# Optimization experiments

Hardware: AMD Instinct MI355X
Metric: run time of the kernel (lower is better)

## Reference

```python
import jax, jax.numpy as jnp
import numpy as np

B, S, D, H = 2, 2048, 1024, 16
HD = D // H  # head_dim = 64


def setup_inputs() -> dict:
    key = jax.random.key(0)
    ks = jax.random.split(key, 5)
    scale = 1.0 / np.sqrt(D)  # xavier-ish init scale
    return {
        "x": jax.random.normal(ks[0], (B, S, D), jnp.float32),
        "Wq": jax.random.normal(ks[1], (D, D), jnp.float32) * scale,
        "Wk": jax.random.normal(ks[2], (D, D), jnp.float32) * scale,
        "Wv": jax.random.normal(ks[3], (D, D), jnp.float32) * scale,
        "Wo": jax.random.normal(ks[4], (D, D), jnp.float32) * scale,
        "bo": jnp.zeros((D,), jnp.float32),
    }


def reference(x, Wq, Wk, Wv, Wo, bo):
    # nn.Linear stores weight as [out, in]; y = x @ W.T
    b, s, d = x.shape
    def heads(t):
        return t.reshape(b, s, H, HD).transpose(0, 2, 1, 3)  # [B,H,S,HD]
    Q = heads(x @ Wq.T)
    K = heads(x @ Wk.T)
    V = heads(x @ Wv.T)
    # Chunked loop in the original sees all K per Q-chunk => full attention.
    scores = jnp.einsum("bhqd,bhkd->bhqk", Q, K) / np.sqrt(HD)
    attn = jax.nn.softmax(scores, axis=-1)
    out = jnp.einsum("bhqk,bhkd->bhqd", attn, V)
    out = out.transpose(0, 2, 1, 3).reshape(b, s, d)
    return out @ Wo.T + bo
```

## Files before the change

kernel.cpp:

```cpp
#include <hip/hip_runtime.h>
#include <hip/hip_bf16.h>
#include <math.h>

#define Bc 2
#define Sc 2048
#define Dc 1024
#define Hc 16
#define HDc 64
#define Mc (Bc*Sc)

using f32x4  = __attribute__((ext_vector_type(4))) float;
using bf16x8 = __attribute__((ext_vector_type(8))) short;
using s16x4  = __attribute__((ext_vector_type(4))) short;
using uint4v = __attribute__((ext_vector_type(4))) unsigned int;

#define GAS(p) ((const __attribute__((address_space(1))) void*)(p))
#define LAS(p) ((__attribute__((address_space(3))) void*)(p))

#define QSC 0.18033688011112042f

__device__ __forceinline__ short f2b(float f) {
  union { float f; unsigned u; } v; v.f = f;
  unsigned r = (v.u + 0x7fffu + ((v.u >> 16) & 1u)) >> 16;
  return (short)r;
}

__global__ __launch_bounds__(256) void cvt_kernel(const float* __restrict__ in,
                                                  short* __restrict__ out, int n4) {
  int i = blockIdx.x * 256 + threadIdx.x;
  if (i >= n4) return;
  float4 v = reinterpret_cast<const float4*>(in)[i];
  s16x4 o;
  o.x = f2b(v.x); o.y = f2b(v.y); o.z = f2b(v.z); o.w = f2b(v.w);
  reinterpret_cast<s16x4*>(out)[i] = o;
}

__global__ __launch_bounds__(256) void cvtw_kernel(
    const float* __restrict__ w0, const float* __restrict__ w1,
    const float* __restrict__ w2, const float* __restrict__ w3,
    short* __restrict__ o0, short* __restrict__ o1,
    short* __restrict__ o2, short* __restrict__ o3) {
  const int sel = blockIdx.y;
  const float* in = (sel == 0) ? w0 : (sel == 1) ? w1 : (sel == 2) ? w2 : w3;
  short* out = (sel == 0) ? o0 : (sel == 1) ? o1 : (sel == 2) ? o2 : o3;
  int i = blockIdx.x * 256 + threadIdx.x;
  float4 v = reinterpret_cast<const float4*>(in)[i];
  s16x4 o;
  o.x = f2b(v.x); o.y = f2b(v.y); o.z = f2b(v.z); o.w = f2b(v.w);
  reinterpret_cast<s16x4*>(out)[i] = o;
}

__device__ __forceinline__ void gemm_core_128(
    const short* __restrict__ A, const short* __restrict__ Bt,
    int m0, int n0, short* As, short* Bs, f32x4 (&acc)[4][4]) {
  const int tid = threadIdx.x;
  const int l = tid & 63;
  const int w = tid >> 6;
  const int wr = w >> 1, wc = w & 1;
  const int g = l >> 4;

  int srow[4], scol[4];
#pragma unroll
  for (int i = 0; i < 4; ++i) {
    int off = w * 1024 + i * 4096 + l * 16;
    int row = off >> 7;
    srow[i] = row;
    scol[i] = (off & 127) ^ ((row & 7) << 4);
  }
  const int rA = (wr * 64 + (l & 15)) * 128;
  const int rB = (wc * 64 + (l & 15)) * 128;
  const int sw = (l & 7) << 4;

  for (int kt = 0; kt < 16; ++kt) {
#pragma unroll
    for (int i = 0; i < 4; ++i) {
      const char* ga = (const char*)A + (size_t)(m0 + srow[i]) * 2048 + kt * 128 + scol[i];
      const char* gb = (const char*)Bt + (size_t)(n0 + srow[i]) * 2048 + kt * 128 + scol[i];
      __builtin_amdgcn_global_load_lds(GAS(ga), LAS((char*)As + w * 1024 + i * 4096), 16, 0, 0);
      __builtin_amdgcn_global_load_lds(GAS(gb), LAS((char*)Bs + w * 1024 + i * 4096), 16, 0, 0);
    }
    __syncthreads();
#pragma unroll
    for (int ks = 0; ks < 2; ++ks) {
      bf16x8 af[4], bfr[4];
#pragma unroll
      for (int mi = 0; mi < 4; ++mi)
        af[mi] = *(const bf16x8*)((const char*)As + rA + mi * 2048 + ((g * 16 + ks * 64) ^ sw));
#pragma unroll
      for (int ni = 0; ni < 4; ++ni)
        bfr[ni] = *(const bf16x8*)((const char*)Bs + rB + ni * 2048 + ((g * 16 + ks * 64) ^ sw));
#pragma unroll
      for (int mi = 0; mi < 4; ++mi)
#pragma unroll
        for (int ni = 0; ni < 4; ++ni)
          acc[mi][ni] = __builtin_amdgcn_mfma_f32_16x16x32_bf16(af[mi], bfr[ni], acc[mi][ni], 0, 0, 0);
    }
    __syncthreads();
  }
}

__global__ __launch_bounds__(256) void qkv_kernel(
    const short* __restrict__ xb, const short* __restrict__ wq,
    const short* __restrict__ wk, const short* __restrict__ wv,
    short* __restrict__ Qb, short* __restrict__ Kb, short* __restrict__ Vb) {
  __shared__ short As[128 * 64];
  __shared__ short Bs[128 * 64];
  const int mt = blockIdx.x, yb = blockIdx.y;
  const int sel = yb >> 3, nb = yb & 7;
  const short* Wt = (sel == 0) ? wq : (sel == 1) ? wk : wv;
  short* Ob = (sel == 0) ? Qb : (sel == 1) ? Kb : Vb;
  const float oscale = (sel == 0) ? QSC : 1.0f;
  f32x4 acc[4][4];
#pragma unroll
  for (int i = 0; i < 4; ++i)
#pragma unroll
    for (int j = 0; j < 4; ++j)
#pragma unroll
      for (int r = 0; r < 4; ++r) acc[i][j][r] = 0.0f;
  gemm_core_128(xb, Wt, mt * 128, nb * 128, As, Bs, acc);
  const int l = threadIdx.x & 63, w = threadIdx.x >> 6;
  const int wr = w >> 1, wc = w & 1, g = l >> 4;
#pragma unroll
  for (int mi = 0; mi < 4; ++mi)
#pragma unroll
    for (int ni = 0; ni < 4; ++ni) {
      int n = nb * 128 + wc * 64 + ni * 16 + (l & 15);
      int h = n >> 6, hd = n & 63;
#pragma unroll
      for (int r = 0; r < 4; ++r) {
        int m = mt * 128 + wr * 64 + mi * 16 + g * 4 + r;
        int b = m >> 11, s = m & 2047;
        Ob[((size_t)(b * 16 + h) * 2048 + s) * 64 + hd] = f2b(acc[mi][ni][r] * oscale);
      }
    }
}

__global__ __launch_bounds__(256) void oproj_kernel(
    const short* __restrict__ ab, const short* __restrict__ wo,
    const float* __restrict__ bo, float* __restrict__ out) {
  __shared__ short As[128 * 64];
  __shared__ short Bs[128 * 64];
  const int mt = blockIdx.x, nb = blockIdx.y;
  f32x4 acc[4][4];
#pragma unroll
  for (int i = 0; i < 4; ++i)
#pragma unroll
    for (int j = 0; j < 4; ++j)
#pragma unroll
      for (int r = 0; r < 4; ++r) acc[i][j][r] = 0.0f;
  gemm_core_128(ab, wo, mt * 128, nb * 128, As, Bs, acc);
  const int l = threadIdx.x & 63, w = threadIdx.x >> 6;
  const int wr = w >> 1, wc = w & 1, g = l >> 4;
#pragma unroll
  for (int mi = 0; mi < 4; ++mi)
#pragma unroll
    for (int ni = 0; ni < 4; ++ni) {
      int n = nb * 128 + wc * 64 + ni * 16 + (l & 15);
      float bias = bo[n];
#pragma unroll
      for (int r = 0; r < 4; ++r) {
        int m = mt * 128 + wr * 64 + mi * 16 + g * 4 + r;
        out[(size_t)m * 1024 + n] = acc[mi][ni][r] + bias;
      }
    }
}

__global__ __launch_bounds__(256) void vtrans_kernel(const short* __restrict__ Vb,
                                                     short* __restrict__ Vtg) {
  __shared__ short T[64 * 65];
  const int bh = blockIdx.x, st = blockIdx.y;
  const int t = threadIdx.x;
  const short* src = Vb + (size_t)bh * Sc * HDc + (size_t)st * 64 * 64;
#pragma unroll
  for (int i = 0; i < 2; ++i) {
    int r = (t >> 3) + i * 32;
    int c8 = (t & 7) * 8;
    bf16x8 v = *(const bf16x8*)(src + r * 64 + c8);
#pragma unroll
    for (int j = 0; j < 8; ++j) T[r * 65 + c8 + j] = v[j];
  }
  __syncthreads();
  short* dst = Vtg + (size_t)bh * Sc * HDc + st * 64;
#pragma unroll
  for (int i = 0; i < 2; ++i) {
    int hd = (t >> 3) + i * 32;
    int s8 = (t & 7) * 8;
    bf16x8 v;
#pragma unroll
    for (int j = 0; j < 8; ++j) v[j] = T[(s8 + j) * 65 + hd];
    *(bf16x8*)(dst + (size_t)hd * Sc + s8) = v;
  }
}

__global__ __launch_bounds__(256, 2) void attn_kernel(
    const short* __restrict__ Qb, const short* __restrict__ Kb,
    const short* __restrict__ Vtg, short* __restrict__ ab) {
  __shared__ short Ks[3][64 * 64];
  __shared__ short Vs[3][64 * 64];
  const int bh = blockIdx.x;
  const int qt = blockIdx.y;
  const int tid = threadIdx.x, l = tid & 63, w = tid >> 6, g = l >> 4, c = l & 15;
  const int sw = (l & 7) << 4;
  const short* Qp = Qb + (size_t)bh * Sc * HDc;
  const char* KpB = (const char*)(Kb + (size_t)bh * Sc * HDc);
  const char* VtB = (const char*)(Vtg + (size_t)bh * Sc * HDc);
  const int q0 = qt * 128 + w * 32;

  bf16x8 bq[2][2];
#pragma unroll
  for (int qf = 0; qf < 2; ++qf)
#pragma unroll
    for (int ks = 0; ks < 2; ++ks)
      bq[qf][ks] = *(const bf16x8*)(Qp + (size_t)(q0 + qf * 16 + c) * 64 + ks * 32 + g * 8);

  f32x4 o[2][4];
  float lsum[2] = {0.0f, 0.0f};
#pragma unroll
  for (int qf = 0; qf < 2; ++qf)
#pragma unroll
    for (int ohf = 0; ohf < 4; ++ohf)
#pragma unroll
      for (int r = 0; r < 4; ++r) o[qf][ohf][r] = 0.0f;

  size_t koff[2], voff[2];
  int ldst[2];
#pragma unroll
  for (int i = 0; i < 2; ++i) {
    int off = w * 1024 + i * 4096 + l * 16;
    int row = off >> 7;
    int col = (off & 127) ^ ((row & 7) << 4);
    koff[i] = (size_t)row * 128 + col;
    voff[i] = (size_t)row * 4096 + col;
    ldst[i] = w * 1024 + i * 4096;
  }

#define ISSUE3(t_) do {                                                               \
    int b_ = (t_) % 3;                                                                \
    const char* kb_ = KpB + (size_t)(t_) * 8192;                                      \
    const char* vb_ = VtB + (size_t)(t_) * 128;                                       \
    __builtin_amdgcn_global_load_lds(GAS(kb_ + koff[0]), LAS((char*)Ks[b_] + ldst[0]), 16, 0, 0); \
    __builtin_amdgcn_global_load_lds(GAS(kb_ + koff[1]), LAS((char*)Ks[b_] + ldst[1]), 16, 0, 0); \
    __builtin_amdgcn_global_load_lds(GAS(vb_ + voff[0]), LAS((char*)Vs[b_] + ldst[0]), 16, 0, 0); \
    __builtin_amdgcn_global_load_lds(GAS(vb_ + voff[1]), LAS((char*)Vs[b_] + ldst[1]), 16, 0, 0); \
  } while (0)

  ISSUE3(0);
  ISSUE3(1);

  for (int t = 0; t < 32; ++t) {
    if (t < 31) {
      asm volatile("s_waitcnt vmcnt(4)" ::: "memory");
    } else {
      asm volatile("s_waitcnt vmcnt(0)" ::: "memory");
    }
    __builtin_amdgcn_s_barrier();
    if (t < 30) ISSUE3(t + 2);

    const int buf = t % 3;
    const char* KsB = (const char*)Ks[buf];
    const char* VsB = (const char*)Vs[buf];

    bf16x8 ak[2][4], av[2][4];
#pragma unroll
    for (int ks = 0; ks < 2; ++ks)
#pragma unroll
      for (int kf = 0; kf < 4; ++kf) {
        int row = kf * 16 + c;
        ak[ks][kf] = *(const bf16x8*)(KsB + row * 128 + ((ks * 64 + g * 16) ^ sw));
        av[ks][kf] = *(const bf16x8*)(VsB + row * 128 + ((ks * 64 + g * 16) ^ sw));
      }

    f32x4 s[2][4];
#pragma unroll
    for (int qf = 0; qf < 2; ++qf)
#pragma unroll
      for (int kf = 0; kf < 4; ++kf)
#pragma unroll
        for (int r = 0; r < 4; ++r) s[qf][kf][r] = 0.0f;
    __builtin_amdgcn_s_setprio(1);
#pragma unroll
    for (int ks = 0; ks < 2; ++ks)
#pragma unroll
      for (int qf = 0; qf < 2; ++qf)
#pragma unroll
        for (int kf = 0; kf < 4; ++kf)
          s[qf][kf] = __builtin_amdgcn_mfma_f32_16x16x32_bf16(ak[ks][kf], bq[qf][ks], s[qf][kf], 0, 0, 0);
    __builtin_amdgcn_s_setprio(0);

    bf16x8 pb[2][2];
#pragma unroll
    for (int qf = 0; qf < 2; ++qf) {
      float p[4][4];
#pragma unroll
      for (int kf = 0; kf < 4; ++kf)
#pragma unroll
        for (int r = 0; r < 4; ++r)
          p[kf][r] = __builtin_amdgcn_exp2f(s[qf][kf][r]);
      float t0 = (p[0][0] + p[0][1]) + (p[0][2] + p[0][3]);
      float t1 = (p[1][0] + p[1][1]) + (p[1][2] + p[1][3]);
      float t2 = (p[2][0] + p[2][1]) + (p[2][2] + p[2][3]);
      float t3 = (p[3][0] + p[3][1]) + (p[3][2] + p[3][3]);
      lsum[qf] += (t0 + t1) + (t2 + t3);

      unsigned dw[4][2];
#pragma unroll
      for (int kf = 0; kf < 4; ++kf)
#pragma unroll
        for (int d = 0; d < 2; ++d)
          asm("v_cvt_pk_bf16_f32 %0, %1, %2" : "=v"(dw[kf][d]) : "v"(p[kf][2 * d]), "v"(p[kf][2 * d + 1]));

      const bool godd = (l & 16) != 0;
#pragma unroll
      for (int ks2 = 0; ks2 < 2; ++ks2) {
        unsigned T[4];
#pragma unroll
        for (int d = 0; d < 2; ++d) {
          unsigned Av = dw[2 * ks2][d], Bv = dw[2 * ks2 + 1][d];
          asm("v_permlane32_swap_b32 %0, %1" : "+v"(Av), "+v"(Bv));
          unsigned sAv = (unsigned)__shfl_xor((int)Av, 16);
          unsigned sBv = (unsigned)__shfl_xor((int)Bv, 16);
          T[d]     = godd ? sBv : Av;
          T[d + 2] = godd ? Bv  : sAv;
        }
        uint4v t4; t4.x = T[0]; t4.y = T[1]; t4.z = T[2]; t4.w = T[3];
        pb[qf][ks2] = __builtin_bit_cast(bf16x8, t4);
      }
    }

    __builtin_amdgcn_s_setprio(1);
#pragma unroll
    for (int ks2 = 0; ks2 < 2; ++ks2)
#pragma unroll
      for (int ohf = 0; ohf < 4; ++ohf) {
        o[0][ohf] = __builtin_amdgcn_mfma_f32_16x16x32_bf16(av[ks2][ohf], pb[0][ks2], o[0][ohf], 0, 0, 0);
        o[1][ohf] = __builtin_amdgcn_mfma_f32_16x16x32_bf16(av[ks2][ohf], pb[1][ks2], o[1][ohf], 0, 0, 0);
      }
    __builtin_amdgcn_s_setprio(0);
  }

  const int b = bh >> 4, h = bh & 15;
#pragma unroll
  for (int qf = 0; qf < 2; ++qf) {
    float lv = lsum[qf];
    lv += __shfl_xor(lv, 16);
    lv += __shfl_xor(lv, 32);
    float inv = 1.0f / lv;
    int q = q0 + qf * 16 + c;
    short* dst = ab + (size_t)(b * Sc + q) * Dc + h * 64 + g * 4;
#pragma unroll
    for (int ohf = 0; ohf < 4; ++ohf) {
      s16x4 pk4;
#pragma unroll
      for (int r = 0; r < 4; ++r) pk4[r] = f2b(o[qf][ohf][r] * inv);
      *(s16x4*)(dst + ohf * 16) = pk4;
    }
  }
}

extern "C" void kernel_launch(void* const* d_in, const int* in_sizes, int n_in,
                              void* d_out, int out_size, void* d_ws, size_t ws_size,
                              hipStream_t stream) {
  const float* x  = (const float*)d_in[0];
  const float* Wq = (const float*)d_in[1];
  const float* Wk = (const float*)d_in[2];
  const float* Wv = (const float*)d_in[3];
  const float* Wo = (const float*)d_in[4];
  const float* bo = (const float*)d_in[5];
  float* out = (float*)d_out;

  char* p = (char*)d_ws;
  short* xb    = (short*)p; p += (size_t)Mc * Dc * 2;
  short* wqb   = (short*)p; p += (size_t)Dc * Dc * 2;
  short* wkb   = (short*)p; p += (size_t)Dc * Dc * 2;
  short* wvb   = (short*)p; p += (size_t)Dc * Dc * 2;
  short* wob   = (short*)p; p += (size_t)Dc * Dc * 2;
  short* Qb    = (short*)p; p += (size_t)Mc * Dc * 2;
  short* Kb    = (short*)p; p += (size_t)Mc * Dc * 2;
  short* Vb    = (short*)p; p += (size_t)Mc * Dc * 2;
  short* Vtg   = (short*)p; p += (size_t)Mc * Dc * 2;
  short* attnb = (short*)p; p += (size_t)Mc * Dc * 2;

  cvt_kernel<<<(Mc * Dc / 4) / 256, 256, 0, stream>>>(x, xb, Mc * Dc / 4);
  cvtw_kernel<<<dim3((Dc * Dc / 4) / 256, 4), 256, 0, stream>>>(Wq, Wk, Wv, Wo, wqb, wkb, wvb, wob);

  qkv_kernel<<<dim3(Mc / 128, 24), 256, 0, stream>>>(xb, wqb, wkb, wvb, Qb, Kb, Vb);
  vtrans_kernel<<<dim3(Bc * Hc, Sc / 64), 256, 0, stream>>>(Vb, Vtg);
  attn_kernel<<<dim3(Bc * Hc, Sc / 128), 256, 0, stream>>>(Qb, Kb, Vtg, attnb);
  oproj_kernel<<<dim3(Mc / 128, Dc / 128), 256, 0, stream>>>(attnb, wob, bo, out);
}
```

Measured before the change: 200.6 us.

## Split attention KV tile across wave pairs with LDS reduction of partial outputs

The attention block grows from 4 to 8 waves, and each pair of waves shares a 32-row query group while each wave handles half of every 64-key tile. Each wave computes fewer scores and half of the P·V accumulation. The halves are combined at the end through LDS, summing the partial outputs and row sums before normalising. The aim is more waves in flight to hide latency and less work per wave, at the cost of extra barriers, an LDS reduction epilogue and tighter register limits from launch_bounds(512,4).

```diff
diff --git a/kernel.cpp b/kernel.cpp
--- a/kernel.cpp
+++ b/kernel.cpp
@@ -192,19 +192,21 @@
   }
 }
 
-__global__ __launch_bounds__(256, 2) void attn_kernel(
+__global__ __launch_bounds__(512, 4) void attn_kernel(
     const short* __restrict__ Qb, const short* __restrict__ Kb,
     const short* __restrict__ Vtg, short* __restrict__ ab) {
-  __shared__ short Ks[3][64 * 64];
-  __shared__ short Vs[3][64 * 64];
+  __shared__ char lds[49152];
   const int bh = blockIdx.x;
   const int qt = blockIdx.y;
-  const int tid = threadIdx.x, l = tid & 63, w = tid >> 6, g = l >> 4, c = l & 15;
+  const int tid = threadIdx.x, l = tid & 63, w = tid >> 6;
+  const int qg = w >> 1, h = w & 1;
+  const int g = l >> 4, c = l & 15;
   const int sw = (l & 7) << 4;
+  const bool godd = (l & 16) != 0;
   const short* Qp = Qb + (size_t)bh * Sc * HDc;
   const char* KpB = (const char*)(Kb + (size_t)bh * Sc * HDc);
   const char* VtB = (const char*)(Vtg + (size_t)bh * Sc * HDc);
-  const int q0 = qt * 128 + w * 32;
+  const int q0 = qt * 128 + qg * 32;
 
   bf16x8 bq[2][2];
 #pragma unroll
@@ -222,26 +224,18 @@
 #pragma unroll
       for (int r = 0; r < 4; ++r) o[qf][ohf][r] = 0.0f;
 
-  size_t koff[2], voff[2];
-  int ldst[2];
-#pragma unroll
-  for (int i = 0; i < 2; ++i) {
-    int off = w * 1024 + i * 4096 + l * 16;
-    int row = off >> 7;
-    int col = (off & 127) ^ ((row & 7) << 4);
-    koff[i] = (size_t)row * 128 + col;
-    voff[i] = (size_t)row * 4096 + col;
-    ldst[i] = w * 1024 + i * 4096;
-  }
+  const int soff = w * 1024 + l * 16;
+  const int srow = soff >> 7;
+  const int scol = (soff & 127) ^ ((srow & 7) << 4);
+  const size_t koff = (size_t)srow * 128 + scol;
+  const size_t voff = (size_t)srow * 4096 + scol;
+  const int ldst = w * 1024;
 
 #define ISSUE3(t_) do {                                                               \
-    int b_ = (t_) % 3;                                                                \
-    const char* kb_ = KpB + (size_t)(t_) * 8192;                                      \
-    const char* vb_ = VtB + (size_t)(t_) * 128;                                       \
-    __builtin_amdgcn_global_load_lds(GAS(kb_ + koff[0]), LAS((char*)Ks[b_] + ldst[0]), 16, 0, 0); \
-    __builtin_amdgcn_global_load_lds(GAS(kb_ + koff[1]), LAS((char*)Ks[b_] + ldst[1]), 16, 0, 0); \
-    __builtin_amdgcn_global_load_lds(GAS(vb_ + voff[0]), LAS((char*)Vs[b_] + ldst[0]), 16, 0, 0); \
-    __builtin_amdgcn_global_load_lds(GAS(vb_ + voff[1]), LAS((char*)Vs[b_] + ldst[1]), 16, 0, 0); \
+    char* kd_ = lds + ((t_) % 3) * 8192 + ldst;                                       \
+    char* vd_ = lds + 24576 + ((t_) % 3) * 8192 + ldst;                               \
+    __builtin_amdgcn_global_load_lds(GAS(KpB + (size_t)(t_) * 8192 + koff), LAS(kd_), 16, 0, 0); \
+    __builtin_amdgcn_global_load_lds(GAS(VtB + (size_t)(t_) * 128  + voff), LAS(vd_), 16, 0, 0); \
   } while (0)
 
   ISSUE3(0);
@@ -249,111 +243,131 @@
 
   for (int t = 0; t < 32; ++t) {
     if (t < 31) {
-      asm volatile("s_waitcnt vmcnt(4)" ::: "memory");
+      asm volatile("s_waitcnt vmcnt(2)" ::: "memory");
     } else {
       asm volatile("s_waitcnt vmcnt(0)" ::: "memory");
     }
     __builtin_amdgcn_s_barrier();
     if (t < 30) ISSUE3(t + 2);
 
-    const int buf = t % 3;
-    const char* KsB = (const char*)Ks[buf];
-    const char* VsB = (const char*)Vs[buf];
-
-    bf16x8 ak[2][4], av[2][4];
-#pragma unroll
-    for (int ks = 0; ks < 2; ++ks)
-#pragma unroll
-      for (int kf = 0; kf < 4; ++kf) {
-        int row = kf * 16 + c;
-        ak[ks][kf] = *(const bf16x8*)(KsB + row * 128 + ((ks * 64 + g * 16) ^ sw));
-        av[ks][kf] = *(const bf16x8*)(VsB + row * 128 + ((ks * 64 + g * 16) ^ sw));
-      }
-
-    f32x4 s[2][4];
+    const char* KsB = lds + (t % 3) * 8192;
+    const char* VsB = lds + 24576 + (t % 3) * 8192;
+
+    f32x4 s[2][2];
 #pragma unroll
     for (int qf = 0; qf < 2; ++qf)
 #pragma unroll
-      for (int kf = 0; kf < 4; ++kf)
-#pragma unroll
-        for (int r = 0; r < 4; ++r) s[qf][kf][r] = 0.0f;
-    __builtin_amdgcn_s_setprio(1);
-#pragma unroll
-    for (int ks = 0; ks < 2; ++ks)
+      for (int kf2 = 0; kf2 < 2; ++kf2)
+#pragma unroll
+        for (int r = 0; r < 4; ++r) s[qf][kf2][r] = 0.0f;
+#pragma unroll
+    for (int ks = 0; ks < 2; ++ks) {
+      bf16x8 ak[2];
+#pragma unroll
+      for (int kf2 = 0; kf2 < 2; ++kf2) {
+        int row = (2 * h + kf2) * 16 + c;
+        ak[kf2] = *(const bf16x8*)(KsB + row * 128 + ((ks * 64 + g * 16) ^ sw));
+      }
+      __builtin_amdgcn_s_setprio(1);
 #pragma unroll
       for (int qf = 0; qf < 2; ++qf)
 #pragma unroll
-        for (int kf = 0; kf < 4; ++kf)
-          s[qf][kf] = __builtin_amdgcn_mfma_f32_16x16x32_bf16(ak[ks][kf], bq[qf][ks], s[qf][kf], 0, 0, 0);
-    __builtin_amdgcn_s_setprio(0);
-
-    bf16x8 pb[2][2];
+        for (int kf2 = 0; kf2 < 2; ++kf2)
+          s[qf][kf2] = __builtin_amdgcn_mfma_f32_16x16x32_bf16(ak[kf2], bq[qf][ks], s[qf][kf2], 0, 0, 0);
+      __builtin_amdgcn_s_setprio(0);
+    }
+
+    bf16x8 pb[2];
 #pragma unroll
     for (int qf = 0; qf < 2; ++qf) {
-      float p[4][4];
-#pragma unroll
-      for (int kf = 0; kf < 4; ++kf)
+      float p[2][4];
+#pragma unroll
+      for (int kf2 = 0; kf2 < 2; ++kf2)
 #pragma unroll
         for (int r = 0; r < 4; ++r)
-          p[kf][r] = __builtin_amdgcn_exp2f(s[qf][kf][r]);
+          p[kf2][r] = __builtin_amdgcn_exp2f(s[qf][kf2][r]);
       float t0 = (p[0][0] + p[0][1]) + (p[0][2] + p[0][3]);
       float t1 = (p[1][0] + p[1][1]) + (p[1][2] + p[1][3]);
-      float t2 = (p[2][0] + p[2][1]) + (p[2][2] + p[2][3]);
-      float t3 = (p[3][0] + p[3][1]) + (p[3][2] + p[3][3]);
-      lsum[qf] += (t0 + t1) + (t2 + t3);
-
-      unsigned dw[4][2];
-#pragma unroll
-      for (int kf = 0; kf < 4; ++kf)
+      lsum[qf] += t0 + t1;
+
+      unsigned dw[2][2];
+#pragma unroll
+      for (int kf2 = 0; kf2 < 2; ++kf2)
 #pragma unroll
         for (int d = 0; d < 2; ++d)
-          asm("v_cvt_pk_bf16_f32 %0, %1, %2" : "=v"(dw[kf][d]) : "v"(p[kf][2 * d]), "v"(p[kf][2 * d + 1]));
-
-      const bool godd = (l & 16) != 0;
-#pragma unroll
-      for (int ks2 = 0; ks2 < 2; ++ks2) {
-        unsigned T[4];
-#pragma unroll
-        for (int d = 0; d < 2; ++d) {
-          unsigned Av = dw[2 * ks2][d], Bv = dw[2 * ks2 + 1][d];
-          asm("v_permlane32_swap_b32 %0, %1" : "+v"(Av), "+v"(Bv));
-          unsigned sAv = (unsigned)__shfl_xor((int)Av, 16);
-          unsigned sBv = (unsigned)__shfl_xor((int)Bv, 16);
-          T[d]     = godd ? sBv : Av;
-          T[d + 2] = godd ? Bv  : sAv;
+          asm("v_cvt_pk_bf16_f32 %0, %1, %2" : "=v"(dw[kf2][d]) : "v"(p[kf2][2 * d]), "v"(p[kf2][2 * d + 1]));
+
+      unsigned T[4];
+#pragma unroll
+      for (int d = 0; d < 2; ++d) {
+        unsigned Av = dw[0][d], Bv = dw[1][d];
+        asm("v_permlane32_swap_b32 %0, %1" : "+v"(Av), "+v"(Bv));
+        unsigned sAv = (unsigned)__shfl_xor((int)Av, 16);
+        unsigned sBv = (unsigned)__shfl_xor((int)Bv, 16);
+        T[d]     = godd ? sBv : Av;
+        T[d + 2] = godd ? Bv  : sAv;
+      }
+      uint4v t4; t4.x = T[0]; t4.y = T[1]; t4.z = T[2]; t4.w = T[3];
+      pb[qf] = __builtin_bit_cast(bf16x8, t4);
+    }
+
+    {
+      bf16x8 av[4];
+#pragma unroll
+      for (int ohf = 0; ohf < 4; ++ohf) {
+        int row = ohf * 16 + c;
+        av[ohf] = *(const bf16x8*)(VsB + row * 128 + ((h * 64 + g * 16) ^ sw));
+      }
+      __builtin_amdgcn_s_setprio(1);
+#pragma unroll
+      for (int ohf = 0; ohf < 4; ++ohf) {
+        o[0][ohf] = __builtin_amdgcn_mfma_f32_16x16x32_bf16(av[ohf], pb[0], o[0][ohf], 0, 0, 0);
+        o[1][ohf] = __builtin_amdgcn_mfma_f32_16x16x32_bf16(av[ohf], pb[1], o[1][ohf], 0, 0, 0);
+      }
+      __builtin_amdgcn_s_setprio(0);
+    }
+  }
+
+  float* So = (float*)lds;
+  float* Sl = (float*)(lds + 24576);
+  const int b = bh >> 4, hh = bh & 15;
+  float lv[2];
+
+  __syncthreads();
+#pragma unroll
+  for (int qf = 0; qf < 2; ++qf) {
+    if (h == 1) {
+#pragma unroll
+      for (int ohf = 0; ohf < 4; ++ohf)
+        *(f32x4*)(So + qg * 1024 + l * 16 + ohf * 4) = o[qf][ohf];
+      if (qf == 0) {
+        Sl[qg * 128 + l * 2 + 0] = lsum[0];
+        Sl[qg * 128 + l * 2 + 1] = lsum[1];
+      }
+    }
+    __syncthreads();
+    if (h == 0) {
+      if (qf == 0) {
+#pragma unroll
+        for (int j = 0; j < 2; ++j) {
+          float lt = lsum[j] + Sl[qg * 128 + l * 2 + j];
+          lt += __shfl_xor(lt, 16);
+          lt += __shfl_xor(lt, 32);
+          lv[j] = 1.0f / lt;
         }
-        uint4v t4; t4.x = T[0]; t4.y = T[1]; t4.z = T[2]; t4.w = T[3];
-        pb[qf][ks2] = __builtin_bit_cast(bf16x8, t4);
-      }
-    }
-
-    __builtin_amdgcn_s_setprio(1);
-#pragma unroll
-    for (int ks2 = 0; ks2 < 2; ++ks2)
+      }
+      int q = q0 + qf * 16 + c;
+      short* dst = ab + (size_t)(b * Sc + q) * Dc + hh * 64 + g * 4;
 #pragma unroll
       for (int ohf = 0; ohf < 4; ++ohf) {
-        o[0][ohf] = __builtin_amdgcn_mfma_f32_16x16x32_bf16(av[ks2][ohf], pb[0][ks2], o[0][ohf], 0, 0, 0);
-        o[1][ohf] = __builtin_amdgcn_mfma_f32_16x16x32_bf16(av[ks2][ohf], pb[1][ks2], o[1][ohf], 0, 0, 0);
-      }
-    __builtin_amdgcn_s_setprio(0);
-  }
-
-  const int b = bh >> 4, h = bh & 15;
-#pragma unroll
-  for (int qf = 0; qf < 2; ++qf) {
-    float lv = lsum[qf];
-    lv += __shfl_xor(lv, 16);
-    lv += __shfl_xor(lv, 32);
-    float inv = 1.0f / lv;
-    int q = q0 + qf * 16 + c;
-    short* dst = ab + (size_t)(b * Sc + q) * Dc + h * 64 + g * 4;
-#pragma unroll
-    for (int ohf = 0; ohf < 4; ++ohf) {
-      s16x4 pk4;
-#pragma unroll
-      for (int r = 0; r < 4; ++r) pk4[r] = f2b(o[qf][ohf][r] * inv);
-      *(s16x4*)(dst + ohf * 16) = pk4;
-    }
+        f32x4 om = o[qf][ohf] + *(const f32x4*)(So + qg * 1024 + l * 16 + ohf * 4);
+        s16x4 pk4;
+#pragma unroll
+        for (int r = 0; r < 4; ++r) pk4[r] = f2b(om[r] * lv[qf]);
+        *(s16x4*)(dst + ohf * 16) = pk4;
+      }
+    }
+    __syncthreads();
   }
 }
 
@@ -385,6 +399,6 @@
 
   qkv_kernel<<<dim3(Mc / 128, 24), 256, 0, stream>>>(xb, wqb, wkb, wvb, Qb, Kb, Vb);
   vtrans_kernel<<<dim3(Bc * Hc, Sc / 64), 256, 0, stream>>>(Vb, Vtg);
-  attn_kernel<<<dim3(Bc * Hc, Sc / 128), 256, 0, stream>>>(Qb, Kb, Vtg, attnb);
+  attn_kernel<<<dim3(Bc * Hc, Sc / 128), 512, 0, stream>>>(Qb, Kb, Vtg, attnb);
   oproj_kernel<<<dim3(Mc / 128, Dc / 128), 256, 0, stream>>>(attnb, wob, bo, out);
 }
```

Measured after the change: 196.1 us. 2.3% less time.
